# Kernel optimization log

Hardware: AMD Instinct MI355X
Metric: run time of the kernel (lower is better)

## Reference

```python
import jax, jax.numpy as jnp
import numpy as np

H, DV, DM = 16, 64, 1024   # n_head, d_v, d_model
B, L = 8, 1024             # batch, seq len (len_k == len_v)
LN_EPS = 1e-5


def setup_inputs() -> dict:
    key = jax.random.key(0)
    ks = jax.random.split(key, 8)
    rn = lambda i, shape, scale=1.0: (jax.random.normal(ks[i], shape, jnp.float32) * scale)
    return {
        "q": rn(0, (B, L, DM)),
        "k": rn(1, (B, L, DM)),
        "v": rn(2, (B, L, DM)),
        "posi_att": rn(3, (H, L, L), 0.1),
        "w_k": rn(4, (H, DM), float(np.sqrt(2.0 / (DM + 1)))),
        "b_k": jnp.zeros((H,), jnp.float32),
        "w_v": rn(5, (H * DV, DM), float(np.sqrt(2.0 / (DM + DV)))),
        "b_v": jnp.zeros((H * DV,), jnp.float32),
        "w_fc": rn(6, (DM, H * DV), float(np.sqrt(2.0 / (DM + H * DV)))),
        "b_fc": jnp.zeros((DM,), jnp.float32),
        "ln_g": jnp.ones((DM,), jnp.float32),
        "ln_b": jnp.zeros((DM,), jnp.float32),
    }


def reference(q, k, v, posi_att, w_k, b_k, w_v, b_v, w_fc, b_fc, ln_g, ln_b):
    # q is unused by the original forward (only its device is read)
    b, l, _ = k.shape
    # key projection: d_k == 1, so one scalar per (token, head)
    kk = k @ w_k.T + b_k                               # [b, l, H]
    vv = (v @ w_v.T + b_v).reshape(b, l, H, DV)        # [b, l, H, DV]
    # temperature = sqrt(d_k) = 1.0 -> no-op, kept for faithfulness
    kk = kk / 1.0
    # scores[h, b, i, j] = kk[b, i, h] + posi_att[h, i, j]  (head-major, matches torch view)
    scores = kk.transpose(2, 0, 1)[..., None] + posi_att[:, None, :, :]  # [H, b, l, l]
    diag = jnp.eye(l, dtype=bool)
    scores = jnp.where(diag, -jnp.inf, scores)
    attn = jax.nn.softmax(scores, axis=-1)             # [H, b, l, l]
    # dropout is identity in eval mode
    out = jnp.einsum('hbqk,bkhd->bqhd', attn, vv).reshape(b, l, H * DV)
    out = out @ w_fc.T + b_fc                          # [b, l, DM]
    mu = out.mean(-1, keepdims=True)
    var = out.var(-1, keepdims=True)
    out = (out - mu) / jnp.sqrt(var + LN_EPS) * ln_g + ln_b
    return out, attn.reshape(H * b, l, l)
```

## Files before the change

### kernel.cpp

```cpp
#include <hip/hip_runtime.h>
#include <stdint.h>

#define NH 16
#define NDV 64
#define NDM 1024
#define NB 8
#define NL 1024

typedef __attribute__((ext_vector_type(8))) short short8;
typedef __attribute__((ext_vector_type(4))) short short4v;
typedef __attribute__((ext_vector_type(4))) float f32x4;

static __device__ __forceinline__ unsigned short f2bf(float x) {
    unsigned int u = __builtin_bit_cast(unsigned int, x);
    unsigned int r = (u + 0x7fffu + ((u >> 16) & 1u)) >> 16;
    return (unsigned short)r;
}

static __device__ __forceinline__ float waveMax(float v) {
#pragma unroll
    for (int o = 32; o > 0; o >>= 1) v = fmaxf(v, __shfl_xor(v, o, 64));
    return v;
}
static __device__ __forceinline__ float waveSum(float v) {
#pragma unroll
    for (int o = 32; o > 0; o >>= 1) v += __shfl_xor(v, o, 64);
    return v;
}

static __device__ __forceinline__ void gload_lds16(const void* g, void* l) {
    __builtin_amdgcn_global_load_lds((const __attribute__((address_space(1))) void*)g,
                                     (__attribute__((address_space(3))) void*)l, 16, 0, 0);
}

__global__ __launch_bounds__(256) void phaseA(
    const float* __restrict__ posi, float* __restrict__ attn_out,
    unsigned short* __restrict__ a_bf,
    const float* __restrict__ v, const float* __restrict__ wv, const float* __restrict__ wfc,
    unsigned short* __restrict__ v_bf, unsigned short* __restrict__ wv_bf,
    unsigned short* __restrict__ wfc_bf) {
    __shared__ float red[8];
    const int bid = blockIdx.x;
    const int t = threadIdx.x;
    if (bid < 16384) {
        const int h = bid >> 10, i = bid & 1023;
        const float4* rowp = (const float4*)(posi + (((size_t)h << 10) + i) * 1024);
        float4 p = rowp[t];
        const int j0 = t << 2;
        float* pf = (float*)&p;
        if (i >= j0 && i < j0 + 4) pf[i - j0] = -1e30f;
        float m = fmaxf(fmaxf(pf[0], pf[1]), fmaxf(pf[2], pf[3]));
        m = waveMax(m);
        if ((t & 63) == 0) red[t >> 6] = m;
        __syncthreads();
        m = fmaxf(fmaxf(red[0], red[1]), fmaxf(red[2], red[3]));
        const float e0 = __expf(pf[0] - m), e1 = __expf(pf[1] - m);
        const float e2 = __expf(pf[2] - m), e3 = __expf(pf[3] - m);
        float s = waveSum(e0 + e1 + e2 + e3);
        if ((t & 63) == 0) red[4 + (t >> 6)] = s;
        __syncthreads();
        s = red[4] + red[5] + red[6] + red[7];
        const float inv = 1.0f / s;
        f32x4 a;
        a[0] = e0 * inv; a[1] = e1 * inv; a[2] = e2 * inv; a[3] = e3 * inv;
        float* base = attn_out + (((size_t)(h << 3)) << 20) + ((size_t)i << 10);
#pragma unroll
        for (int b = 0; b < 8; ++b)
            __builtin_nontemporal_store(a, (f32x4*)(base + ((size_t)b << 20)) + t);
        short4v u;
        u[0] = (short)f2bf(a[0]); u[1] = (short)f2bf(a[1]);
        u[2] = (short)f2bf(a[2]); u[3] = (short)f2bf(a[3]);
        *(short4v*)(a_bf + ((((size_t)h << 10) + i) << 10) + j0) = u;
    } else {
        int b = bid - 16384;
        const float* src;
        unsigned short* dst;
        if (b < 8192)      { src = v;   dst = v_bf; }
        else if (b < 9216) { src = wv;  dst = wv_bf;  b -= 8192; }
        else               { src = wfc; dst = wfc_bf; b -= 9216; }
        const size_t idx = ((size_t)b * 256 + t) << 2;
        const float4 x = *(const float4*)(src + idx);
        short4v u;
        u[0] = (short)f2bf(x.x); u[1] = (short)f2bf(x.y);
        u[2] = (short)f2bf(x.z); u[3] = (short)f2bf(x.w);
        *(short4v*)(dst + idx) = u;
    }
}

template <int EPI>
static __device__ __forceinline__ void gemm128_core(
    const unsigned short* __restrict__ A,
    const unsigned short* __restrict__ Bt,
    const float* __restrict__ bias,
    void* __restrict__ Cout,
    const int K, const int tm, const int tn, const int bh,
    unsigned short* sA, unsigned short* sB) {
    const int tid = threadIdx.x;
    const int lane = tid & 63;
    const int w = tid >> 6;
    const int wr = w >> 1, wc = w & 1;

    const unsigned short* Ab = A + (size_t)tm * 128 * K;
    const unsigned short* Bb = Bt + (size_t)tn * 128 * K;

    const int lrow = lane >> 3;
    const int lch = lane & 7;

    int offA[2][4], offB[2][4];
#pragma unroll
    for (int ks = 0; ks < 2; ++ks)
#pragma unroll
        for (int f = 0; f < 4; ++f) {
            const int fra = wr * 64 + f * 16 + (lane & 15);
            offA[ks][f] = fra * 64 + ((ks * 4 + (lane >> 4)) ^ (fra & 7)) * 8;
            const int frb = wc * 64 + f * 16 + (lane & 15);
            offB[ks][f] = frb * 64 + ((ks * 4 + (lane >> 4)) ^ (frb & 7)) * 8;
        }

    f32x4 acc[4][4];
#pragma unroll
    for (int i = 0; i < 4; ++i)
#pragma unroll
        for (int j = 0; j < 4; ++j) acc[i][j] = (f32x4){0.f, 0.f, 0.f, 0.f};

    const int nst = K >> 6;

#define STAGE64(buf, kt)                                                          \
    {                                                                             \
        unsigned short* dA = sA + ((buf) << 13);                                  \
        unsigned short* dB = sB + ((buf) << 13);                                  \
        _Pragma("unroll")                                                         \
        for (int g = 0; g < 4; ++g) {                                             \
            const int row = w * 32 + g * 8 + lrow;                                \
            const int sc = ((lch ^ (row & 7)) << 3);                              \
            gload_lds16(Ab + (size_t)row * K + (kt) + sc, dA + (w * 32 + g * 8) * 64); \
            gload_lds16(Bb + (size_t)row * K + (kt) + sc, dB + (w * 32 + g * 8) * 64); \
        }                                                                         \
    }

    STAGE64(0, 0)

    for (int t = 0; t < nst; ++t) {
        __builtin_amdgcn_s_barrier();
        __builtin_amdgcn_sched_barrier(0);
        if (t + 1 < nst) {
            STAGE64((t + 1) & 1, (t + 1) << 6)
            asm volatile("s_waitcnt vmcnt(8)" ::: "memory");
        } else {
            asm volatile("s_waitcnt vmcnt(0)" ::: "memory");
        }
        __builtin_amdgcn_s_barrier();
        __builtin_amdgcn_sched_barrier(0);
        const unsigned short* bA = sA + ((t & 1) << 13);
        const unsigned short* bB = sB + ((t & 1) << 13);
#pragma unroll
        for (int ks = 0; ks < 2; ++ks) {
            short8 af[4], bfv[4];
#pragma unroll
            for (int f = 0; f < 4; ++f) af[f] = *(const short8*)&bA[offA[ks][f]];
#pragma unroll
            for (int f = 0; f < 4; ++f) bfv[f] = *(const short8*)&bB[offB[ks][f]];
            __builtin_amdgcn_s_setprio(1);
#pragma unroll
            for (int i = 0; i < 4; ++i)
#pragma unroll
                for (int j = 0; j < 4; ++j)
                    acc[i][j] = __builtin_amdgcn_mfma_f32_16x16x32_bf16(af[i], bfv[j], acc[i][j], 0, 0, 0);
            __builtin_amdgcn_s_setprio(0);
        }
    }
#undef STAGE64

#pragma unroll
    for (int i = 0; i < 4; ++i) {
        const int gRow0 = tm * 128 + wr * 64 + i * 16 + ((lane >> 4) << 2);
#pragma unroll
        for (int j = 0; j < 4; ++j) {
            const int gCol = tn * 128 + wc * 64 + j * 16 + (lane & 15);
            f32x4 v = acc[i][j];
            if (EPI == 1) {
                const float bb2 = bias[gCol];
                const int hh = gCol >> 6, dd = gCol & 63;
                const int b = gRow0 >> 10, ll2 = gRow0 & 1023;
                unsigned short* C = (unsigned short*)Cout;
                short4v u;
                u[0] = (short)f2bf(v[0] + bb2);
                u[1] = (short)f2bf(v[1] + bb2);
                u[2] = (short)f2bf(v[2] + bb2);
                u[3] = (short)f2bf(v[3] + bb2);
                *(short4v*)(C + (size_t)hh * 524288 + ((size_t)b * 64 + dd) * 1024 + ll2) = u;
            } else if (EPI == 2) {
                const int b = gCol >> 6, dd = gCol & 63;
                unsigned short* X = (unsigned short*)Cout;
#pragma unroll
                for (int r = 0; r < 4; ++r)
                    X[((size_t)b * 1024 + gRow0 + r) * 1024 + bh * 64 + dd] = f2bf(v[r]);
            } else {
                const float bb2 = bias[gCol];
                float* O = (float*)Cout;
#pragma unroll
                for (int r = 0; r < 4; ++r)
                    O[(size_t)(gRow0 + r) * 1024 + gCol] = v[r] + bb2;
            }
        }
    }
}

__global__ __launch_bounds__(256) void gemm_k1(const unsigned short* __restrict__ A,
                                               const unsigned short* __restrict__ Bt,
                                               const float* __restrict__ bias,
                                               unsigned short* __restrict__ C) {
    __shared__ unsigned short sA[16384], sB[16384];
    const int s = (blockIdx.x & 7) * 64 + (blockIdx.x >> 3);
    gemm128_core<1>(A, Bt, bias, C, 1024, s >> 3, s & 7, 0, sA, sB);
}

__global__ __launch_bounds__(256) void gemm_k2(const unsigned short* __restrict__ A,
                                               const unsigned short* __restrict__ Bt,
                                               unsigned short* __restrict__ X) {
    __shared__ unsigned short sA[16384], sB[16384];
    const int s = (blockIdx.x & 7) * 64 + (blockIdx.x >> 3);
    const int bh = s >> 5;
    gemm128_core<2>(A + (size_t)bh * 1048576, Bt + (size_t)bh * 524288, nullptr, X,
                    1024, (s >> 2) & 7, s & 3, bh, sA, sB);
}

__global__ __launch_bounds__(256) void gemm_k3(const unsigned short* __restrict__ A,
                                               const unsigned short* __restrict__ Bt,
                                               const float* __restrict__ bias,
                                               float* __restrict__ O) {
    __shared__ unsigned short sA[16384], sB[16384];
    const int s = (blockIdx.x & 7) * 64 + (blockIdx.x >> 3);
    gemm128_core<3>(A, Bt, bias, O, 1024, s >> 3, s & 7, 0, sA, sB);
}

__global__ __launch_bounds__(256) void ln_kernel(float* __restrict__ out,
                                                 const float* __restrict__ g,
                                                 const float* __restrict__ b) {
    __shared__ float red[8];
    const int row = blockIdx.x, t = threadIdx.x;
    float4* p = (float4*)(out + ((size_t)row << 10));
    float4 x = p[t];
    float s = x.x + x.y + x.z + x.w;
    float sq = x.x * x.x + x.y * x.y + x.z * x.z + x.w * x.w;
    s = waveSum(s);
    sq = waveSum(sq);
    if ((t & 63) == 0) { red[t >> 6] = s; red[4 + (t >> 6)] = sq; }
    __syncthreads();
    s = red[0] + red[1] + red[2] + red[3];
    sq = red[4] + red[5] + red[6] + red[7];
    const float mu = s * (1.f / 1024.f);
    const float var = sq * (1.f / 1024.f) - mu * mu;
    const float rinv = rsqrtf(var + 1e-5f);
    const float4 gg = ((const float4*)g)[t];
    const float4 bb = ((const float4*)b)[t];
    x.x = (x.x - mu) * rinv * gg.x + bb.x;
    x.y = (x.y - mu) * rinv * gg.y + bb.y;
    x.z = (x.z - mu) * rinv * gg.z + bb.z;
    x.w = (x.w - mu) * rinv * gg.w + bb.w;
    p[t] = x;
}

extern "C" void kernel_launch(void* const* d_in, const int* in_sizes, int n_in,
                              void* d_out, int out_size, void* d_ws, size_t ws_size,
                              hipStream_t stream) {
    const float* v    = (const float*)d_in[2];
    const float* posi = (const float*)d_in[3];
    const float* w_v  = (const float*)d_in[6];
    const float* b_v  = (const float*)d_in[7];
    const float* w_fc = (const float*)d_in[8];
    const float* b_fc = (const float*)d_in[9];
    const float* ln_g = (const float*)d_in[10];
    const float* ln_b = (const float*)d_in[11];

    float* out = (float*)d_out;
    float* attn_out = out + (size_t)NB * NL * NDM;

    char* ws = (char*)d_ws;
    unsigned short* A_bf   = (unsigned short*)(ws);
    unsigned short* v_bf   = (unsigned short*)(ws + 33554432);
    unsigned short* wv_bf  = (unsigned short*)(ws + 50331648);
    unsigned short* wfc_bf = (unsigned short*)(ws + 52428800);
    unsigned short* vvT    = (unsigned short*)(ws + 54525952);
    unsigned short* X      = (unsigned short*)(ws + 71303168);

    phaseA<<<26624, 256, 0, stream>>>(posi, attn_out, A_bf, v, w_v, w_fc, v_bf, wv_bf, wfc_bf);
    gemm_k1<<<512, 256, 0, stream>>>(v_bf, wv_bf, b_v, vvT);
    gemm_k2<<<512, 256, 0, stream>>>(A_bf, vvT, X);
    gemm_k3<<<512, 256, 0, stream>>>(X, wfc_bf, b_fc, out);
    ln_kernel<<<8192, 256, 0, stream>>>(out, ln_g, ln_b);
}
```

Baseline: 215.6 us.

## Overlap attention batch replication with GEMM kernels via extra copy waves

phaseA now writes only batch 0 of each attention row, and the other 7 batch copies are produced by two extra waves added to each GEMM block (384 threads). These waves read the stored row and write it to the 7 other batch slots while the GEMM waves compute. The intent is to hide the large attention output write traffic behind the compute-bound GEMMs instead of serialising it in phaseA. The risks are added barrier coupling with the GEMM waves, reduced occupancy from the larger blocks, and extra read traffic.

```diff
diff --git a/kernel.cpp b/kernel.cpp
--- a/kernel.cpp
+++ b/kernel.cpp
@@ -64,9 +64,7 @@
         f32x4 a;
         a[0] = e0 * inv; a[1] = e1 * inv; a[2] = e2 * inv; a[3] = e3 * inv;
         float* base = attn_out + (((size_t)(h << 3)) << 20) + ((size_t)i << 10);
-#pragma unroll
-        for (int b = 0; b < 8; ++b)
-            __builtin_nontemporal_store(a, (f32x4*)(base + ((size_t)b << 20)) + t);
+        ((f32x4*)base)[t] = a;
         short4v u;
         u[0] = (short)f2bf(a[0]); u[1] = (short)f2bf(a[1]);
         u[2] = (short)f2bf(a[2]); u[3] = (short)f2bf(a[3]);
@@ -206,32 +204,57 @@
     }
 }
 
-__global__ __launch_bounds__(256) void gemm_k1(const unsigned short* __restrict__ A,
-                                               const unsigned short* __restrict__ Bt,
-                                               const float* __restrict__ bias,
-                                               unsigned short* __restrict__ C) {
+static __device__ __forceinline__ void rep_waves(float* __restrict__ attn_out,
+                                                 int row0, int nrows) {
+    const int l2 = threadIdx.x - 256;
+    f32x4 c0 = {0.f, 0.f, 0.f, 0.f}, c1 = c0;
+    if (nrows > 0) {
+        const int rr = row0;
+        const float* src = attn_out + (((size_t)((rr >> 10) << 3)) << 20) + ((size_t)(rr & 1023) << 10);
+        c0 = ((const f32x4*)src)[l2];
+        c1 = ((const f32x4*)src)[l2 + 128];
+    }
+    for (int t = 0; t < 16; ++t) {
+        __builtin_amdgcn_s_barrier();
+        f32x4 n0 = c0, n1 = c1;
+        if (t + 1 < nrows) {
+            const int rr = row0 + t + 1;
+            const float* src = attn_out + (((size_t)((rr >> 10) << 3)) << 20) + ((size_t)(rr & 1023) << 10);
+            n0 = ((const f32x4*)src)[l2];
+            n1 = ((const f32x4*)src)[l2 + 128];
+        }
+        if (t < nrows) {
+            const int rr = row0 + t;
+            float* dst = attn_out + (((size_t)((rr >> 10) << 3)) << 20) + ((size_t)(rr & 1023) << 10);
+#pragma unroll
+            for (int b = 1; b < 8; ++b) {
+                __builtin_nontemporal_store(c0, (f32x4*)(dst + ((size_t)b << 20)) + l2);
+                __builtin_nontemporal_store(c1, (f32x4*)(dst + ((size_t)b << 20)) + l2 + 128);
+            }
+        }
+        __builtin_amdgcn_s_barrier();
+        c0 = n0; c1 = n1;
+    }
+}
+
+template <int EPI>
+__global__ __launch_bounds__(384, 3) void gemm_rep(
+    const unsigned short* __restrict__ A, const unsigned short* __restrict__ Bt,
+    const float* __restrict__ bias, void* __restrict__ Cout,
+    float* __restrict__ attn_out, int repBase, int repPerBlk) {
     __shared__ unsigned short sA[16384], sB[16384];
-    const int s = (blockIdx.x & 7) * 64 + (blockIdx.x >> 3);
-    gemm128_core<1>(A, Bt, bias, C, 1024, s >> 3, s & 7, 0, sA, sB);
-}
-
-__global__ __launch_bounds__(256) void gemm_k2(const unsigned short* __restrict__ A,
-                                               const unsigned short* __restrict__ Bt,
-                                               unsigned short* __restrict__ X) {
-    __shared__ unsigned short sA[16384], sB[16384];
-    const int s = (blockIdx.x & 7) * 64 + (blockIdx.x >> 3);
-    const int bh = s >> 5;
-    gemm128_core<2>(A + (size_t)bh * 1048576, Bt + (size_t)bh * 524288, nullptr, X,
-                    1024, (s >> 2) & 7, s & 3, bh, sA, sB);
-}
-
-__global__ __launch_bounds__(256) void gemm_k3(const unsigned short* __restrict__ A,
-                                               const unsigned short* __restrict__ Bt,
-                                               const float* __restrict__ bias,
-                                               float* __restrict__ O) {
-    __shared__ unsigned short sA[16384], sB[16384];
-    const int s = (blockIdx.x & 7) * 64 + (blockIdx.x >> 3);
-    gemm128_core<3>(A, Bt, bias, O, 1024, s >> 3, s & 7, 0, sA, sB);
+    if (threadIdx.x < 256) {
+        const int s = (blockIdx.x & 7) * 64 + (blockIdx.x >> 3);
+        if (EPI == 2) {
+            const int bh = s >> 5;
+            gemm128_core<2>(A + (size_t)bh * 1048576, Bt + (size_t)bh * 524288, bias, Cout,
+                            1024, (s >> 2) & 7, s & 3, bh, sA, sB);
+        } else {
+            gemm128_core<EPI>(A, Bt, bias, Cout, 1024, s >> 3, s & 7, 0, sA, sB);
+        }
+    } else {
+        rep_waves(attn_out, repBase + blockIdx.x * repPerBlk, repPerBlk);
+    }
 }
 
 __global__ __launch_bounds__(256) void ln_kernel(float* __restrict__ out,
@@ -285,8 +308,8 @@
     unsigned short* X      = (unsigned short*)(ws + 71303168);
 
     phaseA<<<26624, 256, 0, stream>>>(posi, attn_out, A_bf, v, w_v, w_fc, v_bf, wv_bf, wfc_bf);
-    gemm_k1<<<512, 256, 0, stream>>>(v_bf, wv_bf, b_v, vvT);
-    gemm_k2<<<512, 256, 0, stream>>>(A_bf, vvT, X);
-    gemm_k3<<<512, 256, 0, stream>>>(X, wfc_bf, b_fc, out);
+    gemm_rep<1><<<512, 384, 0, stream>>>(v_bf, wv_bf, b_v, vvT, attn_out, 0, 11);
+    gemm_rep<2><<<512, 384, 0, stream>>>(A_bf, vvT, nullptr, X, attn_out, 5632, 11);
+    gemm_rep<3><<<512, 384, 0, stream>>>(X, wfc_bf, b_fc, out, attn_out, 11264, 10);
     ln_kernel<<<8192, 256, 0, stream>>>(out, ln_g, ln_b);
 }
```

After: 225.6 us. 1.05x slower.
